# Optimization experiments

Measured on AMD Instinct MI355X. Metric: run time of the kernel, lower is better.

Reference implementation:

```python
import jax, jax.numpy as jnp
import numpy as np

MIN_SCALE = 0.05  # module's current_tide default

def setup_inputs() -> dict:
    key = jax.random.key(0)
    k1, k2, k3, k4 = jax.random.split(key, 4)
    B, T, D, N = 8, 2048, 512, 4096
    x = jax.random.normal(k1, (B, T, D), dtype=jnp.float32)
    positions = jax.random.normal(k2, (N, D), dtype=jnp.float32) * 0.5
    values = jax.random.normal(k3, (N, D), dtype=jnp.float32) * 0.02
    temperature = jax.random.uniform(k4, (N,), dtype=jnp.float32)
    frozen_scale = jnp.ones((N,), dtype=jnp.float32)
    frozen = jnp.ones((N,), dtype=bool)
    return {"x": x, "positions": positions, "values": values,
            "temperature": temperature, "frozen_scale": frozen_scale,
            "frozen": frozen}

def reference(x, positions, values, temperature, frozen_scale, frozen):
    B, T, D = x.shape
    xf = x.reshape(-1, D)  # [B*T, D]
    # Euclidean cdist via ||a||^2 + ||b||^2 - 2 a.b
    d2 = (jnp.sum(xf * xf, axis=-1, keepdims=True)
          + jnp.sum(positions * positions, axis=-1)[None, :]
          - 2.0 * (xf @ positions.T))
    dists = jnp.sqrt(jnp.maximum(d2, 0.0))  # [B*T, N]
    effective_scale = jnp.where(frozen, frozen_scale, jnp.float32(MIN_SCALE))
    effective_temp = (jnp.abs(temperature) + 0.1) * effective_scale  # [N]
    weights = jnp.exp(-dists / effective_temp[None, :])
    weights = weights / (jnp.sum(weights, axis=-1, keepdims=True) + 1e-8)
    out = weights @ values  # [B*T, D]
    return out.reshape(B, T, D)
```

## Files before the change

### kernel.cpp

```cpp
#include <hip/hip_runtime.h>
#include <math.h>

static constexpr int D    = 512;
static constexpr int NPOS = 4096;
static constexpr int M    = 16384;
static constexpr float MIN_SCALE = 0.05f;

typedef unsigned short u16;
typedef __attribute__((ext_vector_type(8)))  short short8_t;
typedef __attribute__((ext_vector_type(16))) float f32x16_t;
typedef __attribute__((ext_vector_type(8)))  unsigned short ushort8_t;

__device__ __forceinline__ u16 f2bf(float f) {
    unsigned u = __float_as_uint(f);
    unsigned r = (u + 0x7FFFu + ((u >> 16) & 1u)) >> 16;
    return (u16)r;
}
__device__ __forceinline__ float bf2f(u16 h) {
    return __uint_as_float(((unsigned)h) << 16);
}
__device__ __forceinline__ void async16(void* lds, const void* gp) {
    __builtin_amdgcn_global_load_lds(
        (const __attribute__((address_space(1))) unsigned int*)gp,
        (__attribute__((address_space(3))) unsigned int*)lds, 16, 0, 0);
}


__global__ __launch_bounds__(256) void pre_kernel(
    const float* __restrict__ x, const float* __restrict__ pos,
    const float* __restrict__ val, const float* __restrict__ temperature,
    const float* __restrict__ frozen_scale, const int* __restrict__ frozen,
    float* __restrict__ ws_f, u16* __restrict__ pb3, u16* __restrict__ vt3,
    u16* __restrict__ xb3)
{
    const int b   = blockIdx.x;
    const int tid = threadIdx.x;

    if (b < 1024) {
        const int wv = tid >> 6, lane = tid & 63;
        const int n  = b * 4 + wv;
        const float* row = pos + (size_t)n * D;
        float s = 0.f;
        #pragma unroll
        for (int q = 0; q < D; q += 64) { float v = row[q + lane]; s += v * v; }
        #pragma unroll
        for (int off = 32; off > 0; off >>= 1) s += __shfl_down(s, off, 64);
        if (lane == 0) {
            ws_f[n] = s;
            float es = (frozen[n] != 0) ? frozen_scale[n] : MIN_SCALE;
            float et = (fabsf(temperature[n]) + 0.1f) * es;
            ws_f[NPOS + n] = -1.0f / et;
        }
    } else if (b < 5120) {
        const int wv = tid >> 6, lane = tid & 63;
        const int m  = (b - 1024) * 4 + wv;
        const float* row = x + (size_t)m * D;
        float s = 0.f;
        #pragma unroll
        for (int q = 0; q < D; q += 64) { float v = row[q + lane]; s += v * v; }
        #pragma unroll
        for (int off = 32; off > 0; off >>= 1) s += __shfl_down(s, off, 64);
        if (lane == 0) ws_f[2 * NPOS + m] = s;
    } else if (b < 9216) {
        const size_t f = (size_t)(b - 5120) * 256 + tid;
        const int lane = (int)(f & 63);
        const int kg   = (int)((f >> 6) & 31);
        const int mg   = (int)(f >> 11);
        const float* src = x + ((size_t)(mg * 32 + (lane & 31)) * D
                                + kg * 16 + (lane >> 5) * 8);
        const float4 a = *(const float4*)src;
        const float4 c = *(const float4*)(src + 4);
        ushort8_t v;
        v[0]=f2bf(a.x); v[1]=f2bf(a.y); v[2]=f2bf(a.z); v[3]=f2bf(a.w);
        v[4]=f2bf(c.x); v[5]=f2bf(c.y); v[6]=f2bf(c.z); v[7]=f2bf(c.w);
        *(ushort8_t*)(xb3 + f * 8) = v;
    } else if (b < 10240) {
        const size_t f = (size_t)(b - 9216) * 256 + tid;
        const int lane = (int)(f & 63);
        const int kg   = (int)((f >> 6) & 31);
        const int ng   = (int)(f >> 11);
        const float* src = pos + ((size_t)(ng * 32 + (lane & 31)) * D
                                  + kg * 16 + (lane >> 5) * 8);
        const float4 a = *(const float4*)src;
        const float4 c = *(const float4*)(src + 4);
        ushort8_t v;
        v[0]=f2bf(a.x); v[1]=f2bf(a.y); v[2]=f2bf(a.z); v[3]=f2bf(a.w);
        v[4]=f2bf(c.x); v[5]=f2bf(c.y); v[6]=f2bf(c.z); v[7]=f2bf(c.w);
        *(ushort8_t*)(pb3 + f * 8) = v;
    } else {
        __shared__ __attribute__((aligned(16))) float tile[64 * 68];
        const int b2 = b - 10240;
        const int n0 = (b2 & 63) * 64, d0 = (b2 >> 6) * 64;
        {
            const int row = tid >> 2, c0 = (tid & 3) * 16;
            const float* src = val + (size_t)(n0 + row) * D + d0 + c0;
            #pragma unroll
            for (int i = 0; i < 4; ++i)
                *(float4*)&tile[row * 68 + c0 + i * 4] = *(const float4*)(src + i * 4);
        }
        __syncthreads();
        #pragma unroll
        for (int ff = 0; ff < 2; ++ff) {
            const int f    = ff * 256 + tid;
            const int lane = f & 63;
            const int kgl  = (f >> 6) & 3;
            const int dgl  = (f >> 8) & 1;
            const int d_loc = dgl * 32 + (lane & 31);
            const int n_base = kgl * 16 + (lane >> 5) * 8;
            ushort8_t v;
            #pragma unroll
            for (int c = 0; c < 8; ++c) v[c] = f2bf(tile[(n_base + c) * 68 + d_loc]);
            const int dg = (d0 >> 5) + dgl;
            const int kga = (n0 >> 4) + kgl;
            *(ushort8_t*)(vt3 + ((size_t)(dg * 256 + kga) * 64 + lane) * 8) = v;
        }
    }
}

__global__ __launch_bounds__(1024, 4) void tidal_main(
    const float* __restrict__ ws_f, const u16* __restrict__ pb3,
    const u16* __restrict__ vt3, const u16* __restrict__ xb3,
    float* __restrict__ out)
{
    __shared__ __attribute__((aligned(16))) u16 XBL[2][32][512];
    __shared__ __attribute__((aligned(16))) u16 WTF[2][16][512];
    __shared__ float red[2][8][32];
    __shared__ float inv_s[64];

    const float* pn_arr = ws_f;
    const float* it_arr = ws_f + NPOS;
    const float* xn_arr = ws_f + 2 * NPOS;

    const int tid  = threadIdx.x;
    const int lane = tid & 63;
    const int wave = tid >> 6;
    const int h    = lane >> 5;
    const int l31  = lane & 31;
    const int mh   = wave & 1;
    const int wq   = wave >> 1;
    const int m0   = blockIdx.x * 64;

    {
        const u16* xb_blk = xb3 + (size_t)blockIdx.x * (2 * 32 * 512);
        #pragma unroll
        for (int s = 0; s < 4; ++s) {
            const int seg = wave * 4 + s;
            async16(&XBL[0][0][0] + seg * 512, xb_blk + (size_t)seg * 512 + lane * 8);
        }
    }
    __syncthreads();

    const float xn_r = xn_arr[m0 + mh * 32 + l31];

    f32x16_t O0 = (f32x16_t)0.f, O1 = (f32x16_t)0.f;
    float den_r = 0.f;

    for (int tile = 0; tile < NPOS / 256; ++tile) {
        const int n0 = tile * 256;

        f32x16_t S = (f32x16_t)0.f;
        const u16* pbw = pb3 + (size_t)(tile * 8 + wq) * 32 * 512;
        #pragma unroll 4
        for (int kg = 0; kg < 32; ++kg) {
            const short8_t A = *(const short8_t*)(pbw + (size_t)kg * 512 + lane * 8);
            const short8_t B = *(const short8_t*)&XBL[mh][kg][lane * 8];
            S = __builtin_amdgcn_mfma_f32_32x32x16_bf16(A, B, S, 0, 0, 0);
        }

        #pragma unroll
        for (int t = 0; t < 4; ++t) {
            const int nb = n0 + wq * 32 + 8 * t + 4 * h;
            const float4 pn4 = *(const float4*)(pn_arr + nb);
            const float4 it4 = *(const float4*)(it_arr + nb);
            const float pnv[4] = {pn4.x, pn4.y, pn4.z, pn4.w};
            const float itv[4] = {it4.x, it4.y, it4.z, it4.w};
            u16 hh[4];
            #pragma unroll
            for (int r = 0; r < 4; ++r) {
                const float d2 = xn_r + pnv[r] - 2.f * S[4 * t + r];
                const float w  = __expf(sqrtf(fmaxf(d2, 0.f)) * itv[r]);
                hh[r] = f2bf(w);
                den_r += bf2f(hh[r]);
            }
            u16* dst = &WTF[mh][wq * 2 + (t >> 1)][(l31 + 32 * (t & 1)) * 8 + 4 * h];
            *(unsigned*)(dst)     = (unsigned)hh[0] | ((unsigned)hh[1] << 16);
            *(unsigned*)(dst + 2) = (unsigned)hh[2] | ((unsigned)hh[3] << 16);
        }
        __syncthreads();

        #pragma unroll 4
        for (int nkg = 0; nkg < 16; ++nkg) {
            const int kga = tile * 16 + nkg;
            const short8_t A  = *(const short8_t*)&WTF[mh][nkg][lane * 8];
            const short8_t B0 = *(const short8_t*)(vt3 + ((size_t)(wq * 256 + kga) * 64 + lane) * 8);
            const short8_t B1 = *(const short8_t*)(vt3 + ((size_t)((wq + 8) * 256 + kga) * 64 + lane) * 8);
            O0 = __builtin_amdgcn_mfma_f32_32x32x16_bf16(A, B0, O0, 0, 0, 0);
            O1 = __builtin_amdgcn_mfma_f32_32x32x16_bf16(A, B1, O1, 0, 0, 0);
        }
        __syncthreads();
    }

    den_r += __shfl_xor(den_r, 32, 64);
    if (lane < 32) red[mh][wq][l31] = den_r;
    __syncthreads();
    if (tid < 64) {
        float s = 0.f;
        #pragma unroll
        for (int j = 0; j < 8; ++j) s += red[tid >> 5][j][tid & 31];
        inv_s[tid] = 1.f / (s + 1e-8f);
    }
    __syncthreads();

    #pragma unroll
    for (int t = 0; t < 4; ++t) {
        #pragma unroll
        for (int r = 0; r < 4; ++r) {
            const int mr = 8 * t + 4 * h + r;
            const float iv = inv_s[mh * 32 + mr];
            float* orow = out + (size_t)(m0 + mh * 32 + mr) * D;
            orow[wq * 32 + l31]       = O0[4 * t + r] * iv;
            orow[256 + wq * 32 + l31] = O1[4 * t + r] * iv;
        }
    }
}

extern "C" void kernel_launch(void* const* d_in, const int* in_sizes, int n_in,
                              void* d_out, int out_size, void* d_ws, size_t ws_size,
                              hipStream_t stream) {
    const float* xp  = (const float*)d_in[0];
    const float* pos = (const float*)d_in[1];
    const float* val = (const float*)d_in[2];
    const float* tmp = (const float*)d_in[3];
    const float* fsc = (const float*)d_in[4];
    const int*   frz = (const int*)d_in[5];
    float* outp = (float*)d_out;

    float* ws_f = (float*)d_ws;
    u16*   pb3  = (u16*)((char*)d_ws + 98304);
    u16*   vt3  = (u16*)((char*)d_ws + 4292608);
    u16*   xb3  = (u16*)((char*)d_ws + 8486912);

    pre_kernel<<<10752, 256, 0, stream>>>(xp, pos, val, tmp, fsc, frz,
                                          ws_f, pb3, vt3, xb3);
    tidal_main<<<M / 64, 1024, 0, stream>>>(ws_f, pb3, vt3, xb3, outp);
}
```

Measured before the change: 327.3 us.

## Halve main-kernel waves so each computes two row tiles and reuses operand loads

The main kernel goes from 1024 to 512 threads per block. Each wave now computes both 32-row halves, so every global load of the position and value fragments feeds two MFMAs instead of one. The x tile is streamed into LDS in two K halves to cut LDS use, and the final barrier of each tile is removed. The weight path switches to exp2 with a pre-scaled log2e constant and native sqrt, and the denominator now sums the fp32 weights rather than their bf16-rounded values. The pre-kernel processes several rows per block so it launches fewer blocks. The trade-off is higher register pressure from four output accumulators, and the denominator no longer matches the bf16 weights used in the second matmul exactly.

```diff
diff --git a/kernel.cpp b/kernel.cpp
--- a/kernel.cpp
+++ b/kernel.cpp
@@ -10,14 +10,12 @@
 typedef __attribute__((ext_vector_type(8)))  short short8_t;
 typedef __attribute__((ext_vector_type(16))) float f32x16_t;
 typedef __attribute__((ext_vector_type(8)))  unsigned short ushort8_t;
+typedef __attribute__((ext_vector_type(4)))  unsigned short ushort4_t;
 
 __device__ __forceinline__ u16 f2bf(float f) {
     unsigned u = __float_as_uint(f);
     unsigned r = (u + 0x7FFFu + ((u >> 16) & 1u)) >> 16;
     return (u16)r;
-}
-__device__ __forceinline__ float bf2f(u16 h) {
-    return __uint_as_float(((unsigned)h) << 16);
 }
 __device__ __forceinline__ void async16(void* lds, const void* gp) {
     __builtin_amdgcn_global_load_lds(
@@ -35,61 +33,74 @@
 {
     const int b   = blockIdx.x;
     const int tid = threadIdx.x;
-
-    if (b < 1024) {
-        const int wv = tid >> 6, lane = tid & 63;
-        const int n  = b * 4 + wv;
-        const float* row = pos + (size_t)n * D;
-        float s = 0.f;
-        #pragma unroll
-        for (int q = 0; q < D; q += 64) { float v = row[q + lane]; s += v * v; }
-        #pragma unroll
-        for (int off = 32; off > 0; off >>= 1) s += __shfl_down(s, off, 64);
-        if (lane == 0) {
-            ws_f[n] = s;
-            float es = (frozen[n] != 0) ? frozen_scale[n] : MIN_SCALE;
-            float et = (fabsf(temperature[n]) + 0.1f) * es;
-            ws_f[NPOS + n] = -1.0f / et;
-        }
-    } else if (b < 5120) {
-        const int wv = tid >> 6, lane = tid & 63;
-        const int m  = (b - 1024) * 4 + wv;
-        const float* row = x + (size_t)m * D;
-        float s = 0.f;
-        #pragma unroll
-        for (int q = 0; q < D; q += 64) { float v = row[q + lane]; s += v * v; }
-        #pragma unroll
-        for (int off = 32; off > 0; off >>= 1) s += __shfl_down(s, off, 64);
-        if (lane == 0) ws_f[2 * NPOS + m] = s;
-    } else if (b < 9216) {
-        const size_t f = (size_t)(b - 5120) * 256 + tid;
-        const int lane = (int)(f & 63);
-        const int kg   = (int)((f >> 6) & 31);
-        const int mg   = (int)(f >> 11);
-        const float* src = x + ((size_t)(mg * 32 + (lane & 31)) * D
-                                + kg * 16 + (lane >> 5) * 8);
-        const float4 a = *(const float4*)src;
-        const float4 c = *(const float4*)(src + 4);
-        ushort8_t v;
-        v[0]=f2bf(a.x); v[1]=f2bf(a.y); v[2]=f2bf(a.z); v[3]=f2bf(a.w);
-        v[4]=f2bf(c.x); v[5]=f2bf(c.y); v[6]=f2bf(c.z); v[7]=f2bf(c.w);
-        *(ushort8_t*)(xb3 + f * 8) = v;
-    } else if (b < 10240) {
-        const size_t f = (size_t)(b - 9216) * 256 + tid;
-        const int lane = (int)(f & 63);
-        const int kg   = (int)((f >> 6) & 31);
-        const int ng   = (int)(f >> 11);
-        const float* src = pos + ((size_t)(ng * 32 + (lane & 31)) * D
-                                  + kg * 16 + (lane >> 5) * 8);
-        const float4 a = *(const float4*)src;
-        const float4 c = *(const float4*)(src + 4);
-        ushort8_t v;
-        v[0]=f2bf(a.x); v[1]=f2bf(a.y); v[2]=f2bf(a.z); v[3]=f2bf(a.w);
-        v[4]=f2bf(c.x); v[5]=f2bf(c.y); v[6]=f2bf(c.z); v[7]=f2bf(c.w);
-        *(ushort8_t*)(pb3 + f * 8) = v;
+    const int wv  = tid >> 6, lane = tid & 63;
+
+    if (b < 128) {
+        #pragma unroll
+        for (int i = 0; i < 8; ++i) {
+            const int n = (b * 4 + wv) * 8 + i;
+            const float* row = pos + (size_t)n * D;
+            float s = 0.f;
+            #pragma unroll
+            for (int q = 0; q < D; q += 64) { float v = row[q + lane]; s += v * v; }
+            #pragma unroll
+            for (int off = 32; off > 0; off >>= 1) s += __shfl_down(s, off, 64);
+            if (lane == 0) {
+                ws_f[n] = s;
+                float es = (frozen[n] != 0) ? frozen_scale[n] : MIN_SCALE;
+                float et = (fabsf(temperature[n]) + 0.1f) * es;
+                ws_f[NPOS + n] = -1.4426950408889634f / et;
+            }
+        }
+    } else if (b < 640) {
+        #pragma unroll
+        for (int i = 0; i < 8; ++i) {
+            const int m = ((b - 128) * 4 + wv) * 8 + i;
+            const float* row = x + (size_t)m * D;
+            float s = 0.f;
+            #pragma unroll
+            for (int q = 0; q < D; q += 64) { float v = row[q + lane]; s += v * v; }
+            #pragma unroll
+            for (int off = 32; off > 0; off >>= 1) s += __shfl_down(s, off, 64);
+            if (lane == 0) ws_f[2 * NPOS + m] = s;
+        }
+    } else if (b < 1664) {
+        const int t = (b - 640) * 256 + tid;
+        #pragma unroll
+        for (int rep = 0; rep < 4; ++rep) {
+            const size_t f = (size_t)t + (size_t)rep * 262144;
+            const int l  = (int)(f & 63);
+            const int kg = (int)((f >> 6) & 31);
+            const int mg = (int)(f >> 11);
+            const float* src = x + ((size_t)(mg * 32 + (l & 31)) * D
+                                    + kg * 16 + (l >> 5) * 8);
+            const float4 a = *(const float4*)src;
+            const float4 c = *(const float4*)(src + 4);
+            ushort8_t v;
+            v[0]=f2bf(a.x); v[1]=f2bf(a.y); v[2]=f2bf(a.z); v[3]=f2bf(a.w);
+            v[4]=f2bf(c.x); v[5]=f2bf(c.y); v[6]=f2bf(c.z); v[7]=f2bf(c.w);
+            *(ushort8_t*)(xb3 + f * 8) = v;
+        }
+    } else if (b < 1920) {
+        const int t = (b - 1664) * 256 + tid;
+        #pragma unroll
+        for (int rep = 0; rep < 4; ++rep) {
+            const size_t f = (size_t)t + (size_t)rep * 65536;
+            const int l  = (int)(f & 63);
+            const int kg = (int)((f >> 6) & 31);
+            const int ng = (int)(f >> 11);
+            const float* src = pos + ((size_t)(ng * 32 + (l & 31)) * D
+                                      + kg * 16 + (l >> 5) * 8);
+            const float4 a = *(const float4*)src;
+            const float4 c = *(const float4*)(src + 4);
+            ushort8_t v;
+            v[0]=f2bf(a.x); v[1]=f2bf(a.y); v[2]=f2bf(a.z); v[3]=f2bf(a.w);
+            v[4]=f2bf(c.x); v[5]=f2bf(c.y); v[6]=f2bf(c.z); v[7]=f2bf(c.w);
+            *(ushort8_t*)(pb3 + f * 8) = v;
+        }
     } else {
         __shared__ __attribute__((aligned(16))) float tile[64 * 68];
-        const int b2 = b - 10240;
+        const int b2 = b - 1920;
         const int n0 = (b2 & 63) * 64, d0 = (b2 >> 6) * 64;
         {
             const int row = tid >> 2, c0 = (tid & 3) * 16;
@@ -101,125 +112,145 @@
         __syncthreads();
         #pragma unroll
         for (int ff = 0; ff < 2; ++ff) {
-            const int f    = ff * 256 + tid;
-            const int lane = f & 63;
-            const int kgl  = (f >> 6) & 3;
-            const int dgl  = (f >> 8) & 1;
-            const int d_loc = dgl * 32 + (lane & 31);
-            const int n_base = kgl * 16 + (lane >> 5) * 8;
+            const int fidx = ff * 256 + tid;
+            const int l    = fidx & 63;
+            const int kgl  = (fidx >> 6) & 3;
+            const int dgl  = (fidx >> 8) & 1;
+            const int d_loc  = dgl * 32 + (l & 31);
+            const int n_base = kgl * 16 + (l >> 5) * 8;
             ushort8_t v;
             #pragma unroll
             for (int c = 0; c < 8; ++c) v[c] = f2bf(tile[(n_base + c) * 68 + d_loc]);
-            const int dg = (d0 >> 5) + dgl;
+            const int dg  = (d0 >> 5) + dgl;
             const int kga = (n0 >> 4) + kgl;
-            *(ushort8_t*)(vt3 + ((size_t)(dg * 256 + kga) * 64 + lane) * 8) = v;
-        }
-    }
-}
-
-__global__ __launch_bounds__(1024, 4) void tidal_main(
+            *(ushort8_t*)(vt3 + ((size_t)(dg * 256 + kga) * 64 + l) * 8) = v;
+        }
+    }
+}
+
+__global__ __launch_bounds__(512, 4) void tidal_main(
     const float* __restrict__ ws_f, const u16* __restrict__ pb3,
     const u16* __restrict__ vt3, const u16* __restrict__ xb3,
     float* __restrict__ out)
 {
-    __shared__ __attribute__((aligned(16))) u16 XBL[2][32][512];
-    __shared__ __attribute__((aligned(16))) u16 WTF[2][16][512];
-    __shared__ float red[2][8][32];
+    __shared__ __attribute__((aligned(16))) u16 XBL[32][512];
+    __shared__ __attribute__((aligned(16))) u16 WTF[32][512];
+    __shared__ float red[8][64];
     __shared__ float inv_s[64];
 
-    const float* pn_arr = ws_f;
-    const float* it_arr = ws_f + NPOS;
-    const float* xn_arr = ws_f + 2 * NPOS;
-
-    const int tid  = threadIdx.x;
+    const float* pn_a = ws_f;
+    const float* nl_a = ws_f + NPOS;
+    const float* xn_a = ws_f + 2 * NPOS;
+
+    const int tid = threadIdx.x;
     const int lane = tid & 63;
-    const int wave = tid >> 6;
+    const int wq   = tid >> 6;
     const int h    = lane >> 5;
     const int l31  = lane & 31;
-    const int mh   = wave & 1;
-    const int wq   = wave >> 1;
     const int m0   = blockIdx.x * 64;
 
-    {
-        const u16* xb_blk = xb3 + (size_t)blockIdx.x * (2 * 32 * 512);
-        #pragma unroll
-        for (int s = 0; s < 4; ++s) {
-            const int seg = wave * 4 + s;
-            async16(&XBL[0][0][0] + seg * 512, xb_blk + (size_t)seg * 512 + lane * 8);
-        }
-    }
-    __syncthreads();
-
-    const float xn_r = xn_arr[m0 + mh * 32 + l31];
-
-    f32x16_t O0 = (f32x16_t)0.f, O1 = (f32x16_t)0.f;
-    float den_r = 0.f;
+    const float xn0 = xn_a[m0 + l31];
+    const float xn1 = xn_a[m0 + 32 + l31];
+
+    f32x16_t O00 = (f32x16_t)0.f, O01 = (f32x16_t)0.f;
+    f32x16_t O10 = (f32x16_t)0.f, O11 = (f32x16_t)0.f;
+    float den0 = 0.f, den1 = 0.f;
 
     for (int tile = 0; tile < NPOS / 256; ++tile) {
-        const int n0 = tile * 256;
-
-        f32x16_t S = (f32x16_t)0.f;
-        const u16* pbw = pb3 + (size_t)(tile * 8 + wq) * 32 * 512;
-        #pragma unroll 4
-        for (int kg = 0; kg < 32; ++kg) {
-            const short8_t A = *(const short8_t*)(pbw + (size_t)kg * 512 + lane * 8);
-            const short8_t B = *(const short8_t*)&XBL[mh][kg][lane * 8];
-            S = __builtin_amdgcn_mfma_f32_32x32x16_bf16(A, B, S, 0, 0, 0);
-        }
-
-        #pragma unroll
-        for (int t = 0; t < 4; ++t) {
-            const int nb = n0 + wq * 32 + 8 * t + 4 * h;
-            const float4 pn4 = *(const float4*)(pn_arr + nb);
-            const float4 it4 = *(const float4*)(it_arr + nb);
+        f32x16_t S0 = (f32x16_t)0.f, S1 = (f32x16_t)0.f;
+        const u16* pbw = pb3 + (size_t)((tile * 8 + wq) * 32) * 512;
+
+        #pragma unroll
+        for (int kh = 0; kh < 2; ++kh) {
+            __syncthreads();
+            #pragma unroll
+            for (int s = 0; s < 4; ++s) {
+                const int seg = wq * 4 + s;
+                const int kgl = seg >> 1, mh = seg & 1;
+                const u16* gp = xb3
+                    + (size_t)((2 * blockIdx.x + mh) * 32 + kh * 16 + kgl) * 512
+                    + lane * 8;
+                async16(&XBL[seg][0], gp);
+            }
+            __syncthreads();
+            #pragma unroll 4
+            for (int kgl = 0; kgl < 16; ++kgl) {
+                const short8_t A  = *(const short8_t*)(pbw + (size_t)(kh * 16 + kgl) * 512 + lane * 8);
+                const short8_t B0 = *(const short8_t*)&XBL[kgl * 2 + 0][lane * 8];
+                const short8_t B1 = *(const short8_t*)&XBL[kgl * 2 + 1][lane * 8];
+                S0 = __builtin_amdgcn_mfma_f32_32x32x16_bf16(A, B0, S0, 0, 0, 0);
+                S1 = __builtin_amdgcn_mfma_f32_32x32x16_bf16(A, B1, S1, 0, 0, 0);
+            }
+        }
+
+        #pragma unroll
+        for (int g = 0; g < 4; ++g) {
+            const int nn = 8 * g + 4 * h;
+            const int nb = tile * 256 + wq * 32 + nn;
+            const float4 pn4 = *(const float4*)(pn_a + nb);
+            const float4 nl4 = *(const float4*)(nl_a + nb);
             const float pnv[4] = {pn4.x, pn4.y, pn4.z, pn4.w};
-            const float itv[4] = {it4.x, it4.y, it4.z, it4.w};
-            u16 hh[4];
+            const float nlv[4] = {nl4.x, nl4.y, nl4.z, nl4.w};
+            ushort4_t w0, w1;
             #pragma unroll
             for (int r = 0; r < 4; ++r) {
-                const float d2 = xn_r + pnv[r] - 2.f * S[4 * t + r];
-                const float w  = __expf(sqrtf(fmaxf(d2, 0.f)) * itv[r]);
-                hh[r] = f2bf(w);
-                den_r += bf2f(hh[r]);
-            }
-            u16* dst = &WTF[mh][wq * 2 + (t >> 1)][(l31 + 32 * (t & 1)) * 8 + 4 * h];
-            *(unsigned*)(dst)     = (unsigned)hh[0] | ((unsigned)hh[1] << 16);
-            *(unsigned*)(dst + 2) = (unsigned)hh[2] | ((unsigned)hh[3] << 16);
+                float d2 = fmaxf(fmaf(-2.f, S0[4 * g + r], xn0 + pnv[r]), 0.f);
+                float w  = __builtin_amdgcn_exp2f(__builtin_amdgcn_sqrtf(d2) * nlv[r]);
+                den0 += w; w0[r] = f2bf(w);
+                d2 = fmaxf(fmaf(-2.f, S1[4 * g + r], xn1 + pnv[r]), 0.f);
+                w  = __builtin_amdgcn_exp2f(__builtin_amdgcn_sqrtf(d2) * nlv[r]);
+                den1 += w; w1[r] = f2bf(w);
+            }
+            const int kgn = 2 * wq + (nn >> 4);
+            const int sub = nn & 15;
+            const int h2  = sub >> 3, cb = sub & 7;
+            *(ushort4_t*)&WTF[kgn * 2 + 0][(l31 + 32 * h2) * 8 + cb] = w0;
+            *(ushort4_t*)&WTF[kgn * 2 + 1][(l31 + 32 * h2) * 8 + cb] = w1;
         }
         __syncthreads();
 
-        #pragma unroll 4
-        for (int nkg = 0; nkg < 16; ++nkg) {
-            const int kga = tile * 16 + nkg;
-            const short8_t A  = *(const short8_t*)&WTF[mh][nkg][lane * 8];
-            const short8_t B0 = *(const short8_t*)(vt3 + ((size_t)(wq * 256 + kga) * 64 + lane) * 8);
-            const short8_t B1 = *(const short8_t*)(vt3 + ((size_t)((wq + 8) * 256 + kga) * 64 + lane) * 8);
-            O0 = __builtin_amdgcn_mfma_f32_32x32x16_bf16(A, B0, O0, 0, 0, 0);
-            O1 = __builtin_amdgcn_mfma_f32_32x32x16_bf16(A, B1, O1, 0, 0, 0);
-        }
-        __syncthreads();
-    }
-
-    den_r += __shfl_xor(den_r, 32, 64);
-    if (lane < 32) red[mh][wq][l31] = den_r;
+        const u16* vt0 = vt3 + (size_t)((2 * wq)     * 256 + tile * 16) * 512;
+        const u16* vt1 = vt3 + (size_t)((2 * wq + 1) * 256 + tile * 16) * 512;
+        #pragma unroll 2
+        for (int kg = 0; kg < 16; ++kg) {
+            const short8_t A0 = *(const short8_t*)&WTF[kg * 2 + 0][lane * 8];
+            const short8_t A1 = *(const short8_t*)&WTF[kg * 2 + 1][lane * 8];
+            const short8_t B0 = *(const short8_t*)(vt0 + (size_t)kg * 512 + lane * 8);
+            const short8_t B1 = *(const short8_t*)(vt1 + (size_t)kg * 512 + lane * 8);
+            O00 = __builtin_amdgcn_mfma_f32_32x32x16_bf16(A0, B0, O00, 0, 0, 0);
+            O01 = __builtin_amdgcn_mfma_f32_32x32x16_bf16(A0, B1, O01, 0, 0, 0);
+            O10 = __builtin_amdgcn_mfma_f32_32x32x16_bf16(A1, B0, O10, 0, 0, 0);
+            O11 = __builtin_amdgcn_mfma_f32_32x32x16_bf16(A1, B1, O11, 0, 0, 0);
+        }
+    }
+
+    den0 += __shfl_xor(den0, 32, 64);
+    den1 += __shfl_xor(den1, 32, 64);
+    if (lane < 32) { red[wq][l31] = den0; red[wq][32 + l31] = den1; }
     __syncthreads();
     if (tid < 64) {
-        float s = 0.f;
-        #pragma unroll
-        for (int j = 0; j < 8; ++j) s += red[tid >> 5][j][tid & 31];
-        inv_s[tid] = 1.f / (s + 1e-8f);
+        float s2 = 0.f;
+        #pragma unroll
+        for (int j = 0; j < 8; ++j) s2 += red[j][tid];
+        inv_s[tid] = 1.f / (s2 + 1e-8f);
     }
     __syncthreads();
 
+    const int d0c = 2 * wq * 32 + l31;
+    const int d1c = (2 * wq + 1) * 32 + l31;
     #pragma unroll
-    for (int t = 0; t < 4; ++t) {
+    for (int g = 0; g < 4; ++g) {
         #pragma unroll
         for (int r = 0; r < 4; ++r) {
-            const int mr = 8 * t + 4 * h + r;
-            const float iv = inv_s[mh * 32 + mr];
-            float* orow = out + (size_t)(m0 + mh * 32 + mr) * D;
-            orow[wq * 32 + l31]       = O0[4 * t + r] * iv;
-            orow[256 + wq * 32 + l31] = O1[4 * t + r] * iv;
+            const int mr = r + 8 * g + 4 * h;
+            const float i0 = inv_s[mr];
+            const float i1 = inv_s[32 + mr];
+            float* o0 = out + (size_t)(m0 + mr) * D;
+            float* o1 = out + (size_t)(m0 + 32 + mr) * D;
+            o0[d0c] = O00[4 * g + r] * i0;
+            o0[d1c] = O01[4 * g + r] * i0;
+            o1[d0c] = O10[4 * g + r] * i1;
+            o1[d1c] = O11[4 * g + r] * i1;
         }
     }
 }
@@ -240,7 +271,7 @@
     u16*   vt3  = (u16*)((char*)d_ws + 4292608);
     u16*   xb3  = (u16*)((char*)d_ws + 8486912);
 
-    pre_kernel<<<10752, 256, 0, stream>>>(xp, pos, val, tmp, fsc, frz,
-                                          ws_f, pb3, vt3, xb3);
-    tidal_main<<<M / 64, 1024, 0, stream>>>(ws_f, pb3, vt3, xb3, outp);
-}
+    pre_kernel<<<2432, 256, 0, stream>>>(xp, pos, val, tmp, fsc, frz,
+                                         ws_f, pb3, vt3, xb3);
+    tidal_main<<<M / 64, 512, 0, stream>>>(ws_f, pb3, vt3, xb3, outp);
+}
```

Result: slower. 509.1 us (+55.6%).
